# Kernel optimization log

Hardware: AMD Instinct MI355X
Metric: run time of the kernel (lower is better)

## Reference

```python
import jax, jax.numpy as jnp
import numpy as np

HIDDEN = 1024
HEADS = 16
HEAD_DIM = HIDDEN // HEADS
B, L = 2, 2048
EPS = 1e-5


def setup_inputs() -> dict:
    key = jax.random.key(0)
    ks = jax.random.split(key, 16)
    s = 0.02
    inp = {
        "hidden_state": jax.random.normal(ks[0], (B, L, HIDDEN), jnp.float32),
        "uncertainty_embedding": jax.random.normal(ks[1], (B, HIDDEN), jnp.float32),
        "attention_mask": jnp.ones((B, L), jnp.int32),
        # projection weights stored (in, out): y = x @ W + b
        "Wq": jax.random.normal(ks[2], (HIDDEN, HIDDEN), jnp.float32) * s,
        "bq": jnp.zeros((HIDDEN,), jnp.float32),
        "Wk": jax.random.normal(ks[3], (HIDDEN, HIDDEN), jnp.float32) * s,
        "bk": jnp.zeros((HIDDEN,), jnp.float32),
        "Wv": jax.random.normal(ks[4], (HIDDEN, HIDDEN), jnp.float32) * s,
        "bv": jnp.zeros((HIDDEN,), jnp.float32),
        "Wo": jax.random.normal(ks[5], (HIDDEN, HIDDEN), jnp.float32) * s,
        "bo": jnp.zeros((HIDDEN,), jnp.float32),
        # uncertainty_scale MLP: hidden -> hidden//4 -> num_heads
        "Wu1": jax.random.normal(ks[6], (HIDDEN, HIDDEN // 4), jnp.float32) * s,
        "bu1": jnp.zeros((HIDDEN // 4,), jnp.float32),
        "Wu2": jax.random.normal(ks[7], (HIDDEN // 4, HEADS), jnp.float32) * s,
        "bu2": jnp.zeros((HEADS,), jnp.float32),
        # LayerNorm
        "gamma": jnp.ones((HIDDEN,), jnp.float32),
        "beta": jnp.zeros((HIDDEN,), jnp.float32),
    }
    return inp


def _forward(hidden_state, uncertainty_embedding, attention_mask,
             Wq, bq, Wk, bk, Wv, bv, Wo, bo, Wu1, bu1, Wu2, bu2, gamma, beta):
    Bb, Ll, _ = hidden_state.shape
    # projections -> (B, H, L, Dh)
    def split_heads(x):
        return x.reshape(Bb, Ll, HEADS, HEAD_DIM).transpose(0, 2, 1, 3)
    Q = split_heads(hidden_state @ Wq + bq)
    K = split_heads(hidden_state @ Wk + bk)
    V = split_heads(hidden_state @ Wv + bv)

    scores = jnp.einsum('bhqd,bhkd->bhqk', Q, K) / (HEAD_DIM ** 0.5)
    mask = (attention_mask == 0)[:, None, None, :]  # (B,1,1,L) over key dim
    scores = jnp.where(mask, -1e9, scores)

    # per-head uncertainty gate in (0,1)
    u = jax.nn.relu(uncertainty_embedding @ Wu1 + bu1)
    scale = jax.nn.sigmoid(u @ Wu2 + bu2)  # (B, H)
    scores = scores * scale[:, :, None, None]

    attn = jax.nn.softmax(scores, axis=-1)
    out = jnp.einsum('bhqk,bhkd->bhqd', attn, V)
    out = out.transpose(0, 2, 1, 3).reshape(Bb, Ll, HIDDEN)
    out = out @ Wo + bo

    y = hidden_state + out
    mu = jnp.mean(y, axis=-1, keepdims=True)
    var = jnp.var(y, axis=-1, keepdims=True)
    return (y - mu) * jax.lax.rsqrt(var + EPS) * gamma + beta


def reference(hidden_state, uncertainty_embedding, attention_mask,
              Wq, bq, Wk, bk, Wv, bv, Wo, bo, Wu1, bu1, Wu2, bu2, gamma, beta):
    return _forward(hidden_state, uncertainty_embedding, attention_mask,
                    Wq, bq, Wk, bk, Wv, bv, Wo, bo, Wu1, bu1, Wu2, bu2, gamma, beta)
```

## Files before the change

### kernel.cpp

```cpp
#include <hip/hip_runtime.h>
#include <hip/hip_bf16.h>

#define HID 1024
#define NHEADS 16
#define DH 64
#define BB 2
#define LL 2048
#define MM (BB*LL)
#define EPSF 1e-5f

typedef __attribute__((ext_vector_type(8))) short bf16x8;
typedef __attribute__((ext_vector_type(4))) float f32x4;

#define MFMA16(A,Bf,C) __builtin_amdgcn_mfma_f32_16x16x32_bf16(A,Bf,C,0,0,0)
#define GLOAD_LDS16(G, Ld) \
  __builtin_amdgcn_global_load_lds((__attribute__((address_space(1))) const void*)(G), \
                                   (__attribute__((address_space(3))) void*)(Ld), 16, 0, 0)
#define PIN(v) asm("" : "+v"(v))
#define EXP2R(x) ({ float _y; asm("v_exp_f32 %0, %1" : "=v"(_y) : "v"(x)); _y; })
#define WAIT_VM0_BAR() do { \
    asm volatile("s_waitcnt vmcnt(0)" ::: "memory"); \
    __builtin_amdgcn_s_barrier(); \
    __builtin_amdgcn_sched_barrier(0); \
  } while (0)

__device__ __forceinline__ unsigned short f2bf(float f) {
  union { float f; unsigned int u; } x; x.f = f;
  unsigned int r = x.u + 0x7fffu + ((x.u >> 16) & 1u);
  return (unsigned short)(r >> 16);
}

__global__ __launch_bounds__(256) void u1_partial(const float* __restrict__ ue,
                                                  const float* __restrict__ Wu1,
                                                  float* __restrict__ upart) {
  int b = blockIdx.y, kb = blockIdx.x;
  __shared__ float su[128];
  int tid = threadIdx.x;
  if (tid < 128) su[tid] = ue[b*HID + kb*128 + tid];
  __syncthreads();
  float s = 0.f;
  const float* w = Wu1 + (size_t)(kb*128)*256 + tid;
  for (int k = 0; k < 128; ++k) s += su[k] * w[(size_t)k*256];
  upart[(b*8 + kb)*256 + tid] = s;
}

__global__ __launch_bounds__(256) void u2_scale(const float* __restrict__ upart,
                                                const float* __restrict__ bu1,
                                                const float* __restrict__ Wu2,
                                                const float* __restrict__ bu2,
                                                float* __restrict__ scale) {
  int b = blockIdx.x, tid = threadIdx.x;
  __shared__ float su[256];
  float s = 0.f;
  for (int kb = 0; kb < 8; ++kb) s += upart[(b*8 + kb)*256 + tid];
  su[tid] = fmaxf(s + bu1[tid], 0.f);
  __syncthreads();
  if (tid < 16) {
    float a = bu2[tid];
    for (int k = 0; k < 256; ++k) a += su[k] * Wu2[k*16 + tid];
    scale[b*NHEADS + tid] = 1.f / (1.f + __expf(-a));
  }
}

__global__ __launch_bounds__(256) void maskprep_kernel(const int* __restrict__ amask,
                                                       const float* __restrict__ scale,
                                                       float* __restrict__ maskf) {
  int i = blockIdx.x*256 + threadIdx.x;
  int base = i*8;
  int bh = base >> 11;
  int b  = bh >> 4;
  float cm = scale[bh] * 1.44269504f;
  int k = base & (LL-1);
  #pragma unroll
  for (int j = 0; j < 8; ++j)
    maskf[base + j] = (amask[b*LL + k + j] == 0 ? -1e9f : 0.f) * cm - 16.f;
}

__global__ __launch_bounds__(256) void convert_x_kernel(const float* __restrict__ X,
                                                        unsigned short* __restrict__ Xb) {
  int i = blockIdx.x*256 + threadIdx.x;
  float4 v = ((const float4*)X)[i];
  ushort4 o; o.x = f2bf(v.x); o.y = f2bf(v.y); o.z = f2bf(v.z); o.w = f2bf(v.w);
  ((ushort4*)Xb)[i] = o;
}

__global__ void transw_kernel(const float* __restrict__ Wq, const float* __restrict__ Wk,
                              const float* __restrict__ Wv, const float* __restrict__ Wo,
                              unsigned short* __restrict__ Wqkvt, unsigned short* __restrict__ Wot) {
  __shared__ float tile[32][33];
  int z = blockIdx.z;
  const float* W = (z==0) ? Wq : (z==1) ? Wk : (z==2) ? Wv : Wo;
  unsigned short* dst = (z < 3) ? (Wqkvt + (size_t)z*HID*HID) : Wot;
  int n0 = blockIdx.x*32, k0 = blockIdx.y*32;
  int tx = threadIdx.x, ty = threadIdx.y;
  #pragma unroll
  for (int i = 0; i < 4; ++i) tile[ty+8*i][tx] = W[(size_t)(k0+ty+8*i)*HID + n0+tx];
  __syncthreads();
  #pragma unroll
  for (int i = 0; i < 4; ++i) dst[(size_t)(n0+ty+8*i)*HID + k0+tx] = f2bf(tile[tx][ty+8*i]);
}

template<int MODE>
__global__ __launch_bounds__(256) void gemm_kernel(
    const unsigned short* __restrict__ A,
    const unsigned short* __restrict__ Bt,
    const float* __restrict__ bias0, const float* __restrict__ bias1, const float* __restrict__ bias2,
    const float* __restrict__ resid,
    unsigned short* __restrict__ outQKV,
    float* __restrict__ outY) {
  constexpr int BM = (MODE == 0) ? 128 : 64;
  constexpr int MI = BM / 32;
  constexpr int ASZ = BM*64*2;
  constexpr int BSZ = 128*64*2;
  __shared__ alignas(16) unsigned short sA[2*BM*64];
  __shared__ alignas(16) unsigned short sB[2*128*64];
  const int tid = threadIdx.x, lane = tid & 63, wv = tid >> 6;
  const int wr = wv >> 1, wc = wv & 1;
  const int bid = blockIdx.x, xcd = bid & 7, loc = bid >> 3;
  const int nIdx = (MODE == 0) ? (xcd*3 + loc % 3) : xcd;
  const int mIdx = (MODE == 0) ? (loc / 3) : loc;
  const int m0 = mIdx*BM, n0 = nIdx*128;
  const int r = lane & 15, g = lane >> 4;

  const unsigned short* pA[MI];
  const unsigned short* pB[4];
  int ldsA[MI], ldsB[4];
  #pragma unroll
  for (int c = 0; c < MI; ++c) {
    const int base = c*4096 + wv*1024;
    const int po = base + lane*16;
    const int uo = po ^ (((po>>7)&7)<<4);
    const int e  = uo >> 1;
    pA[c] = A + (size_t)(m0 + (e>>6))*HID + (e&63);
    ldsA[c] = base;
  }
  #pragma unroll
  for (int c = 0; c < 4; ++c) {
    const int base = c*4096 + wv*1024;
    const int po = base + lane*16;
    const int uo = po ^ (((po>>7)&7)<<4);
    const int e  = uo >> 1;
    pB[c] = Bt + (size_t)(n0 + (e>>6))*HID + (e&63);
    ldsB[c] = base;
  }
  const int sw = (r & 7) << 4;
  int oALo = (wr*(MI*16) + r)*128 + ((g*16) ^ sw);
  int oAHi = (wr*(MI*16) + r)*128 + ((64 + g*16) ^ sw);
  int oBLo = (wc*64 + r)*128 + ((g*16) ^ sw);
  int oBHi = (wc*64 + r)*128 + ((64 + g*16) ^ sw);
  PIN(oALo); PIN(oAHi); PIN(oBLo); PIN(oBHi);

#define GSTAGE(BUF) do {                                                      \
    _Pragma("unroll")                                                         \
    for (int c = 0; c < MI; ++c) {                                            \
      GLOAD_LDS16(pA[c], (char*)sA + (BUF)*ASZ + ldsA[c]); pA[c] += 64;       \
    }                                                                         \
    _Pragma("unroll")                                                         \
    for (int c = 0; c < 4; ++c) {                                             \
      GLOAD_LDS16(pB[c], (char*)sB + (BUF)*BSZ + ldsB[c]); pB[c] += 64;       \
    }                                                                         \
  } while (0)

#define GCOMPUTE(BUF) do {                                                    \
    _Pragma("unroll")                                                         \
    for (int kk = 0; kk < 2; ++kk) {                                          \
      bf16x8 af[MI], bfv[4];                                                  \
      _Pragma("unroll")                                                       \
      for (int i = 0; i < MI; ++i)                                            \
        af[i]  = *(const bf16x8*)((const char*)sA + (BUF)*ASZ +               \
                                  (kk ? oAHi : oALo) + i*2048);               \
      _Pragma("unroll")                                                       \
      for (int j = 0; j < 4; ++j)                                             \
        bfv[j] = *(const bf16x8*)((const char*)sB + (BUF)*BSZ +               \
                                  (kk ? oBHi : oBLo) + j*2048);               \
      __builtin_amdgcn_s_setprio(1);                                          \
      _Pragma("unroll")                                                       \
      for (int i = 0; i < MI; ++i)                                            \
        _Pragma("unroll")                                                     \
        for (int j = 0; j < 4; ++j)                                           \
          acc[i][j] = MFMA16(af[i], bfv[j], acc[i][j]);                       \
      __builtin_amdgcn_s_setprio(0);                                          \
    }                                                                         \
  } while (0)

  f32x4 acc[MI][4];
  #pragma unroll
  for (int i = 0; i < MI; ++i)
    #pragma unroll
    for (int j = 0; j < 4; ++j) acc[i][j] = (f32x4){0.f,0.f,0.f,0.f};

  GSTAGE(0);
  for (int k0 = 0; k0 < HID; k0 += 128) {
    WAIT_VM0_BAR();
    GSTAGE(1);
    GCOMPUTE(0);
    WAIT_VM0_BAR();
    if (k0 + 128 < HID) GSTAGE(0);
    GCOMPUTE(1);
  }
#undef GSTAGE
#undef GCOMPUTE

  if (MODE == 0) {
    const int which = n0 >> 10;
    const float* bias = (which==0) ? bias0 : (which==1) ? bias1 : bias2;
    if (which < 2) {
      unsigned short* dst = outQKV + (size_t)which * ((size_t)MM*HID);
      #pragma unroll
      for (int i = 0; i < MI; ++i)
        #pragma unroll
        for (int j = 0; j < 4; ++j)
          #pragma unroll
          for (int rr = 0; rr < 4; ++rr) {
            int row = m0 + wr*(MI*16) + i*16 + g*4 + rr;
            int col = n0 + wc*64 + j*16 + r;
            int nn = col & (HID-1);
            int hh = nn >> 6, d = nn & 63;
            int bI = row >> 11, l = row & (LL-1);
            float v = acc[i][j][rr] + bias[nn];
            dst[(((size_t)(bI*NHEADS + hh)*LL + l) << 6) + d] = f2bf(v);
          }
    } else {
      unsigned short* dst = outQKV + 2*((size_t)MM*HID);
      #pragma unroll
      for (int i = 0; i < MI; ++i)
        #pragma unroll
        for (int j = 0; j < 4; ++j) {
          int col = n0 + wc*64 + j*16 + r;
          int nn = col & (HID-1);
          int hh = nn >> 6, d = nn & 63;
          int row0 = m0 + wr*(MI*16) + i*16 + g*4;
          int bI = row0 >> 11, l0 = row0 & (LL-1);
          ushort4 o4;
          o4.x = f2bf(acc[i][j][0] + bias[nn]);
          o4.y = f2bf(acc[i][j][1] + bias[nn]);
          o4.z = f2bf(acc[i][j][2] + bias[nn]);
          o4.w = f2bf(acc[i][j][3] + bias[nn]);
          *(ushort4*)(dst + ((size_t)((bI*NHEADS + hh)*DH + d))*LL + l0) = o4;
        }
    }
  } else {
    #pragma unroll
    for (int i = 0; i < MI; ++i)
      #pragma unroll
      for (int j = 0; j < 4; ++j)
        #pragma unroll
        for (int rr = 0; rr < 4; ++rr) {
          int row = m0 + wr*(MI*16) + i*16 + g*4 + rr;
          int col = n0 + wc*64 + j*16 + r;
          size_t idx = (size_t)row*HID + col;
          outY[idx] = acc[i][j][rr] + bias0[col] + resid[idx];
        }
  }
}

__global__ __launch_bounds__(256, 4) void attn_kernel(
    const unsigned short* __restrict__ Qb,
    const unsigned short* __restrict__ Kb,
    const unsigned short* __restrict__ Vt,
    const float* __restrict__ maskf,
    const float* __restrict__ scale_ws,
    unsigned short* __restrict__ attnout) {
  __shared__ alignas(16) unsigned short sK[2*64*64];
  __shared__ alignas(16) unsigned short sV[2*64*64];
  __shared__ alignas(16) unsigned short sP[4][16*64];
  const int p = blockIdx.x;
  const int bh = (p & 7)*4 + ((p >> 3) >> 5);
  const int q0 = ((p >> 3) & 31) * 64;
  const int b  = bh >> 4;
  const int tid = threadIdx.x, lane = tid & 63, wv = tid >> 6;
  const int r = lane & 15, g = lane >> 4;
  const size_t hoff = (size_t)bh * (LL*DH);
  const float c2 = 0.125f * scale_ws[bh] * 1.44269504f;
  const unsigned short* Kg = Kb + hoff;
  const unsigned short* Vg = Vt + hoff;
  const float* pm = maskf + (size_t)bh*LL + g*4;

  const unsigned short* pKs[2];
  const unsigned short* pVs[2];
  int lbase[2];
  #pragma unroll
  for (int c = 0; c < 2; ++c) {
    const int base_ = c*4096 + wv*1024;
    const int po_ = base_ + lane*16;
    const int uo_ = po_ ^ (((po_>>7)&7)<<4);
    const int e_  = uo_ >> 1;
    pKs[c] = Kg + (size_t)(e_>>6)*DH + (e_&63);
    pVs[c] = Vg + (size_t)(e_>>6)*LL + (e_&63);
    lbase[c] = base_;
  }

  const int sw = (r & 7) << 4;
  int oLo = r*128 + ((g*16) ^ sw);
  int oHi = r*128 + ((64 + g*16) ^ sw);
  PIN(oLo); PIN(oHi);
  int wP[4];
  #pragma unroll
  for (int kt = 0; kt < 4; ++kt) {
    wP[kt] = r*128 + ((kt*32 + g*8) ^ sw);
    PIN(wP[kt]);
  }

  bf16x8 aQ[2];
  {
    const int qrow = q0 + wv*16 + r;
    #pragma unroll
    for (int kc = 0; kc < 2; ++kc)
      aQ[kc] = *(const bf16x8*)(Qb + hoff + (size_t)qrow*DH + kc*32 + g*8);
  }
  const short ONE_BF = (short)0x3F80;
  const bf16x8 vone = {ONE_BF,ONE_BF,ONE_BF,ONE_BF,ONE_BF,ONE_BF,ONE_BF,ONE_BF};

  f32x4 accO[4];
  #pragma unroll
  for (int j = 0; j < 4; ++j) accO[j] = (f32x4){0.f,0.f,0.f,0.f};
  f32x4 lsum = (f32x4){0.f,0.f,0.f,0.f};

  #pragma unroll
  for (int c = 0; c < 2; ++c) {
    GLOAD_LDS16(pKs[c], (char*)sK + lbase[c]);
    GLOAD_LDS16(pVs[c], (char*)sV + lbase[c]);
    pKs[c] += 64*DH;  pVs[c] += 64;
  }
  float4 mreg[4];
  #pragma unroll
  for (int kt = 0; kt < 4; ++kt) mreg[kt] = *(const float4*)(pm + kt*16);
  pm += 64;

#define ATILE(CUROFF, NBOFF, T) do {                                          \
    WAIT_VM0_BAR();                            \
    if ((T) + 1 < LL/64) {                     \
      _Pragma("unroll")                                                       \
      for (int c = 0; c < 2; ++c) {                                           \
        GLOAD_LDS16(pKs[c], (char*)sK + (NBOFF) + lbase[c]);                  \
        GLOAD_LDS16(pVs[c], (char*)sV + (NBOFF) + lbase[c]);                  \
        pKs[c] += 64*DH;  pVs[c] += 64;                                       \
      }                                                                       \
    }                                                                         \
    f32x4 sc[4];                                                              \
    __builtin_amdgcn_s_setprio(1);                                            \
    _Pragma("unroll")                                                         \
    for (int kt = 0; kt < 4; ++kt) {                                          \
      bf16x8 bk0 = *(const bf16x8*)((const char*)sK + (CUROFF) + oLo + kt*2048); \
      bf16x8 bk1 = *(const bf16x8*)((const char*)sK + (CUROFF) + oHi + kt*2048); \
      f32x4 a = (f32x4){0.f,0.f,0.f,0.f};                                     \
      a = MFMA16(bk0, aQ[0], a);                                              \
      a = MFMA16(bk1, aQ[1], a);                                              \
      sc[kt] = a;                                                             \
    }                                                                         \
    __builtin_amdgcn_s_setprio(0);                                            \
    _Pragma("unroll")                                                         \
    for (int kt = 0; kt < 4; ++kt) {                                          \
      sc[kt][0] = EXP2R(sc[kt][0]*c2 + mreg[kt].x);                           \
      sc[kt][1] = EXP2R(sc[kt][1]*c2 + mreg[kt].y);                           \
      sc[kt][2] = EXP2R(sc[kt][2]*c2 + mreg[kt].z);                           \
      sc[kt][3] = EXP2R(sc[kt][3]*c2 + mreg[kt].w);                           \
    }                                                                         \
    if ((T) + 1 < LL/64) {                                                    \
      _Pragma("unroll")                                                       \
      for (int kt = 0; kt < 4; ++kt) mreg[kt] = *(const float4*)(pm + kt*16); \
      pm += 64;                                                               \
    }                                                                         \
    char* sPw = (char*)sP[wv];                                                \
    _Pragma("unroll")                                                         \
    for (int kt = 0; kt < 4; ++kt) {                                          \
      unsigned int lo, hi;                                                    \
      asm("v_cvt_pk_bf16_f32 %0, %1, %2" : "=v"(lo) : "v"(sc[kt][0]), "v"(sc[kt][1])); \
      asm("v_cvt_pk_bf16_f32 %0, %1, %2" : "=v"(hi) : "v"(sc[kt][2]), "v"(sc[kt][3])); \
      uint2 w; w.x = lo; w.y = hi;                                            \
      *(uint2*)(sPw + wP[kt]) = w;                                            \
    }                                                                         \
    bf16x8 aP0 = *(const bf16x8*)(sPw + oLo);                                 \
    bf16x8 aP1 = *(const bf16x8*)(sPw + oHi);                                 \
    lsum = MFMA16(vone, aP0, lsum);                                           \
    lsum = MFMA16(vone, aP1, lsum);                                           \
    __builtin_amdgcn_s_setprio(1);                                            \
    _Pragma("unroll")                                                         \
    for (int j = 0; j < 4; ++j) {                                             \
      bf16x8 v0 = *(const bf16x8*)((const char*)sV + (CUROFF) + oLo + j*2048); \
      bf16x8 v1 = *(const bf16x8*)((const char*)sV + (CUROFF) + oHi + j*2048); \
      accO[j] = MFMA16(v0, aP0, accO[j]);                                     \
      accO[j] = MFMA16(v1, aP1, accO[j]);                                     \
    }                                                                         \
    __builtin_amdgcn_s_setprio(0);                                            \
  } while (0)

  for (int t = 0; t < LL/64; t += 2) {
    ATILE(0,    8192, t);
    ATILE(8192, 0,    t+1);
  }
#undef ATILE

  const float invl = 1.f / lsum[0];
  const int qq = q0 + wv*16 + r;
  #pragma unroll
  for (int j = 0; j < 4; ++j) {
    ushort4 o4;
    o4.x = f2bf(accO[j][0] * invl);
    o4.y = f2bf(accO[j][1] * invl);
    o4.z = f2bf(accO[j][2] * invl);
    o4.w = f2bf(accO[j][3] * invl);
    const int col = (bh & 15)*DH + j*16 + g*4;
    *(ushort4*)(attnout + (size_t)(b*LL + qq)*HID + col) = o4;
  }
}

__global__ __launch_bounds__(256) void ln_kernel(const float* __restrict__ Y,
                                                 const float* __restrict__ gamma,
                                                 const float* __restrict__ beta,
                                                 float* __restrict__ out) {
  int row = blockIdx.x, tid = threadIdx.x;
  const float* y = Y + (size_t)row*HID;
  float v[4]; float s = 0.f, s2 = 0.f;
  #pragma unroll
  for (int i = 0; i < 4; ++i) { v[i] = y[tid + i*256]; s += v[i]; s2 += v[i]*v[i]; }
  #pragma unroll
  for (int o = 1; o < 64; o <<= 1) { s += __shfl_xor(s, o, 64); s2 += __shfl_xor(s2, o, 64); }
  __shared__ float ws1[4], ws2[4];
  if ((tid & 63) == 0) { ws1[tid>>6] = s; ws2[tid>>6] = s2; }
  __syncthreads();
  s  = ws1[0] + ws1[1] + ws1[2] + ws1[3];
  s2 = ws2[0] + ws2[1] + ws2[2] + ws2[3];
  float mu  = s * (1.f/HID);
  float var = s2 * (1.f/HID) - mu*mu;
  float rs  = rsqrtf(var + EPSF);
  #pragma unroll
  for (int i = 0; i < 4; ++i) {
    int c = tid + i*256;
    out[(size_t)row*HID + c] = (v[i] - mu)*rs*gamma[c] + beta[c];
  }
}

extern "C" void kernel_launch(void* const* d_in, const int* in_sizes, int n_in,
                              void* d_out, int out_size, void* d_ws, size_t ws_size,
                              hipStream_t stream) {
  const float* hidden = (const float*)d_in[0];
  const float* ue     = (const float*)d_in[1];
  const int*   amask  = (const int*)d_in[2];
  const float* Wq = (const float*)d_in[3];  const float* bq = (const float*)d_in[4];
  const float* Wk = (const float*)d_in[5];  const float* bk = (const float*)d_in[6];
  const float* Wv = (const float*)d_in[7];  const float* bv = (const float*)d_in[8];
  const float* Wo = (const float*)d_in[9];  const float* bo = (const float*)d_in[10];
  const float* Wu1 = (const float*)d_in[11]; const float* bu1 = (const float*)d_in[12];
  const float* Wu2 = (const float*)d_in[13]; const float* bu2 = (const float*)d_in[14];
  const float* gamma = (const float*)d_in[15]; const float* beta = (const float*)d_in[16];
  float* out = (float*)d_out;

  char* ws = (char*)d_ws;
  if (ws_size < ((56u<<20) + 32768)) return;
  unsigned short* Xbf   = (unsigned short*)(ws + 0);
  float*          Y     = (float*)(ws + 0);
  float*          maskf = (float*)(ws + (8u<<20));
  unsigned short* Wqkvt = (unsigned short*)(ws + (16u<<20));
  unsigned short* Wot   = (unsigned short*)(ws + (22u<<20));
  unsigned short* Qb    = (unsigned short*)(ws + (24u<<20));
  unsigned short* Kb    = Qb + (size_t)MM*HID;
  unsigned short* Vb    = Kb + (size_t)MM*HID;
  unsigned short* AOut  = (unsigned short*)(ws + (48u<<20));
  float* upart = (float*)(ws + (56u<<20));
  float* scale = upart + BB*8*256;

  u1_partial<<<dim3(8, BB), 256, 0, stream>>>(ue, Wu1, upart);
  u2_scale<<<BB, 256, 0, stream>>>(upart, bu1, Wu2, bu2, scale);
  maskprep_kernel<<<(BB*NHEADS*LL/8)/256, 256, 0, stream>>>(amask, scale, maskf);
  convert_x_kernel<<<(MM*HID/4)/256, 256, 0, stream>>>(hidden, Xbf);
  transw_kernel<<<dim3(32, 32, 4), dim3(32, 8), 0, stream>>>(Wq, Wk, Wv, Wo, Wqkvt, Wot);
  gemm_kernel<0><<<768, 256, 0, stream>>>(Xbf, Wqkvt,
                                          bq, bk, bv, nullptr, Qb, nullptr);
  attn_kernel<<<BB*NHEADS*(LL/64), 256, 0, stream>>>(Qb, Kb, Vb, maskf, scale, AOut);
  gemm_kernel<1><<<512, 256, 0, stream>>>(AOut, Wot,
                                          bo, nullptr, nullptr, hidden, nullptr, Y);
  ln_kernel<<<MM, 256, 0, stream>>>(Y, gamma, beta, out);
}
```

Before: 144.8 us.

## Split attention key tile across waves and feed P directly from registers

Each wave now handles 16 keys of the 64-key tile for all 64 queries, instead of all keys for its own 16 queries. Because the score accumulator layout from the QK MFMA matches the B operand of the 16x16x16 MFMA, P is fed to the PV MFMA straight from registers. This removes the shared-memory P round-trip and the ones-vector MFMA used for row sums. In exchange, the row sums and output accumulators need a multi-barrier cross-wave reduction through LDS at the end, and register pressure grows (launch bounds drop from 4 to 3 blocks per SM).

```diff
diff --git a/kernel.cpp b/kernel.cpp
--- a/kernel.cpp
+++ b/kernel.cpp
@@ -10,9 +10,11 @@
 #define EPSF 1e-5f
 
 typedef __attribute__((ext_vector_type(8))) short bf16x8;
+typedef __attribute__((ext_vector_type(4))) short bf16x4;
 typedef __attribute__((ext_vector_type(4))) float f32x4;
 
 #define MFMA16(A,Bf,C) __builtin_amdgcn_mfma_f32_16x16x32_bf16(A,Bf,C,0,0,0)
+#define MFMA16K16(A,Bf,C) __builtin_amdgcn_mfma_f32_16x16x16bf16_1k(A,Bf,C,0,0,0)
 #define GLOAD_LDS16(G, Ld) \
   __builtin_amdgcn_global_load_lds((__attribute__((address_space(1))) const void*)(G), \
                                    (__attribute__((address_space(3))) void*)(Ld), 16, 0, 0)
@@ -254,7 +256,7 @@
   }
 }
 
-__global__ __launch_bounds__(256, 4) void attn_kernel(
+__global__ __launch_bounds__(256, 3) void attn_kernel(
     const unsigned short* __restrict__ Qb,
     const unsigned short* __restrict__ Kb,
     const unsigned short* __restrict__ Vt,
@@ -263,7 +265,6 @@
     unsigned short* __restrict__ attnout) {
   __shared__ alignas(16) unsigned short sK[2*64*64];
   __shared__ alignas(16) unsigned short sV[2*64*64];
-  __shared__ alignas(16) unsigned short sP[4][16*64];
   const int p = blockIdx.x;
   const int bh = (p & 7)*4 + ((p >> 3) >> 5);
   const int q0 = ((p >> 3) & 31) * 64;
@@ -274,7 +275,7 @@
   const float c2 = 0.125f * scale_ws[bh] * 1.44269504f;
   const unsigned short* Kg = Kb + hoff;
   const unsigned short* Vg = Vt + hoff;
-  const float* pm = maskf + (size_t)bh*LL + g*4;
+  const float* pm = maskf + (size_t)bh*LL + wv*16 + g*4;
 
   const unsigned short* pKs[2];
   const unsigned short* pVs[2];
@@ -291,30 +292,28 @@
   }
 
   const int sw = (r & 7) << 4;
-  int oLo = r*128 + ((g*16) ^ sw);
-  int oHi = r*128 + ((64 + g*16) ^ sw);
-  PIN(oLo); PIN(oHi);
-  int wP[4];
-  #pragma unroll
-  for (int kt = 0; kt < 4; ++kt) {
-    wP[kt] = r*128 + ((kt*32 + g*8) ^ sw);
-    PIN(wP[kt]);
-  }
-
-  bf16x8 aQ[2];
-  {
-    const int qrow = q0 + wv*16 + r;
+  int oKlo = (wv*16 + r)*128 + ((g*16) ^ sw);
+  int oKhi = (wv*16 + r)*128 + ((64 + g*16) ^ sw);
+  int oVb  = r*128 + ((wv*32 + g*8) ^ sw);
+  PIN(oKlo); PIN(oKhi); PIN(oVb);
+
+  bf16x8 aQ[4][2];
+  #pragma unroll
+  for (int qg = 0; qg < 4; ++qg) {
+    const int qrow = q0 + qg*16 + r;
     #pragma unroll
     for (int kc = 0; kc < 2; ++kc)
-      aQ[kc] = *(const bf16x8*)(Qb + hoff + (size_t)qrow*DH + kc*32 + g*8);
-  }
-  const short ONE_BF = (short)0x3F80;
-  const bf16x8 vone = {ONE_BF,ONE_BF,ONE_BF,ONE_BF,ONE_BF,ONE_BF,ONE_BF,ONE_BF};
-
-  f32x4 accO[4];
-  #pragma unroll
-  for (int j = 0; j < 4; ++j) accO[j] = (f32x4){0.f,0.f,0.f,0.f};
-  f32x4 lsum = (f32x4){0.f,0.f,0.f,0.f};
+      aQ[qg][kc] = *(const bf16x8*)(Qb + hoff + (size_t)qrow*DH + kc*32 + g*8);
+  }
+
+  f32x4 accO[4][4];
+  float lp[4];
+  #pragma unroll
+  for (int qg = 0; qg < 4; ++qg) {
+    lp[qg] = 0.f;
+    #pragma unroll
+    for (int j = 0; j < 4; ++j) accO[qg][j] = (f32x4){0.f,0.f,0.f,0.f};
+  }
 
   #pragma unroll
   for (int c = 0; c < 2; ++c) {
@@ -322,10 +321,7 @@
     GLOAD_LDS16(pVs[c], (char*)sV + lbase[c]);
     pKs[c] += 64*DH;  pVs[c] += 64;
   }
-  float4 mreg[4];
-  #pragma unroll
-  for (int kt = 0; kt < 4; ++kt) mreg[kt] = *(const float4*)(pm + kt*16);
-  pm += 64;
+  float4 mreg = *(const float4*)pm;  pm += 64;
 
 #define ATILE(CUROFF, NBOFF, T) do {                                          \
     WAIT_VM0_BAR();                            \
@@ -337,51 +333,43 @@
         pKs[c] += 64*DH;  pVs[c] += 64;                                       \
       }                                                                       \
     }                                                                         \
+    bf16x8 kA0 = *(const bf16x8*)((const char*)sK + (CUROFF) + oKlo);         \
+    bf16x8 kA1 = *(const bf16x8*)((const char*)sK + (CUROFF) + oKhi);         \
+    bf16x4 vA[4];                                                             \
+    _Pragma("unroll")                                                         \
+    for (int j = 0; j < 4; ++j)                                               \
+      vA[j] = *(const bf16x4*)((const char*)sV + (CUROFF) + oVb + j*2048);    \
     f32x4 sc[4];                                                              \
     __builtin_amdgcn_s_setprio(1);                                            \
     _Pragma("unroll")                                                         \
-    for (int kt = 0; kt < 4; ++kt) {                                          \
-      bf16x8 bk0 = *(const bf16x8*)((const char*)sK + (CUROFF) + oLo + kt*2048); \
-      bf16x8 bk1 = *(const bf16x8*)((const char*)sK + (CUROFF) + oHi + kt*2048); \
+    for (int qg = 0; qg < 4; ++qg) {                                          \
       f32x4 a = (f32x4){0.f,0.f,0.f,0.f};                                     \
-      a = MFMA16(bk0, aQ[0], a);                                              \
-      a = MFMA16(bk1, aQ[1], a);                                              \
-      sc[kt] = a;                                                             \
+      a = MFMA16(kA0, aQ[qg][0], a);                                          \
+      a = MFMA16(kA1, aQ[qg][1], a);                                          \
+      sc[qg] = a;                                                             \
     }                                                                         \
     __builtin_amdgcn_s_setprio(0);                                            \
-    _Pragma("unroll")                                                         \
-    for (int kt = 0; kt < 4; ++kt) {                                          \
-      sc[kt][0] = EXP2R(sc[kt][0]*c2 + mreg[kt].x);                           \
-      sc[kt][1] = EXP2R(sc[kt][1]*c2 + mreg[kt].y);                           \
-      sc[kt][2] = EXP2R(sc[kt][2]*c2 + mreg[kt].z);                           \
-      sc[kt][3] = EXP2R(sc[kt][3]*c2 + mreg[kt].w);                           \
+    bf16x4 pb[4];                                                             \
+    _Pragma("unroll")                                                         \
+    for (int qg = 0; qg < 4; ++qg) {                                          \
+      float p0 = EXP2R(sc[qg][0]*c2 + mreg.x);                                \
+      float p1 = EXP2R(sc[qg][1]*c2 + mreg.y);                                \
+      float p2 = EXP2R(sc[qg][2]*c2 + mreg.z);                                \
+      float p3 = EXP2R(sc[qg][3]*c2 + mreg.w);                                \
+      lp[qg] += (p0 + p1) + (p2 + p3);                                        \
+      unsigned int lo, hi;                                                    \
+      asm("v_cvt_pk_bf16_f32 %0, %1, %2" : "=v"(lo) : "v"(p0), "v"(p1));      \
+      asm("v_cvt_pk_bf16_f32 %0, %1, %2" : "=v"(hi) : "v"(p2), "v"(p3));      \
+      unsigned int pw[2] = {lo, hi};                                          \
+      pb[qg] = *(bf16x4*)pw;                                                  \
     }                                                                         \
-    if ((T) + 1 < LL/64) {                                                    \
+    if ((T) + 1 < LL/64) { mreg = *(const float4*)pm;  pm += 64; }            \
+    __builtin_amdgcn_s_setprio(1);                                            \
+    _Pragma("unroll")                                                         \
+    for (int qg = 0; qg < 4; ++qg)                                            \
       _Pragma("unroll")                                                       \
-      for (int kt = 0; kt < 4; ++kt) mreg[kt] = *(const float4*)(pm + kt*16); \
-      pm += 64;                                                               \
-    }                                                                         \
-    char* sPw = (char*)sP[wv];                                                \
-    _Pragma("unroll")                                                         \
-    for (int kt = 0; kt < 4; ++kt) {                                          \
-      unsigned int lo, hi;                                                    \
-      asm("v_cvt_pk_bf16_f32 %0, %1, %2" : "=v"(lo) : "v"(sc[kt][0]), "v"(sc[kt][1])); \
-      asm("v_cvt_pk_bf16_f32 %0, %1, %2" : "=v"(hi) : "v"(sc[kt][2]), "v"(sc[kt][3])); \
-      uint2 w; w.x = lo; w.y = hi;                                            \
-      *(uint2*)(sPw + wP[kt]) = w;                                            \
-    }                                                                         \
-    bf16x8 aP0 = *(const bf16x8*)(sPw + oLo);                                 \
-    bf16x8 aP1 = *(const bf16x8*)(sPw + oHi);                                 \
-    lsum = MFMA16(vone, aP0, lsum);                                           \
-    lsum = MFMA16(vone, aP1, lsum);                                           \
-    __builtin_amdgcn_s_setprio(1);                                            \
-    _Pragma("unroll")                                                         \
-    for (int j = 0; j < 4; ++j) {                                             \
-      bf16x8 v0 = *(const bf16x8*)((const char*)sV + (CUROFF) + oLo + j*2048); \
-      bf16x8 v1 = *(const bf16x8*)((const char*)sV + (CUROFF) + oHi + j*2048); \
-      accO[j] = MFMA16(v0, aP0, accO[j]);                                     \
-      accO[j] = MFMA16(v1, aP1, accO[j]);                                     \
-    }                                                                         \
+      for (int j = 0; j < 4; ++j)                                             \
+        accO[qg][j] = MFMA16K16(vA[j], pb[qg], accO[qg][j]);                  \
     __builtin_amdgcn_s_setprio(0);                                            \
   } while (0)
 
@@ -391,17 +379,73 @@
   }
 #undef ATILE
 
-  const float invl = 1.f / lsum[0];
-  const int qq = q0 + wv*16 + r;
-  #pragma unroll
-  for (int j = 0; j < 4; ++j) {
-    ushort4 o4;
-    o4.x = f2bf(accO[j][0] * invl);
-    o4.y = f2bf(accO[j][1] * invl);
-    o4.z = f2bf(accO[j][2] * invl);
-    o4.w = f2bf(accO[j][3] * invl);
-    const int col = (bh & 15)*DH + j*16 + g*4;
-    *(ushort4*)(attnout + (size_t)(b*LL + qq)*HID + col) = o4;
+  #pragma unroll
+  for (int qg = 0; qg < 4; ++qg) {
+    lp[qg] += __shfl_xor(lp[qg], 16, 64);
+    lp[qg] += __shfl_xor(lp[qg], 32, 64);
+  }
+  __syncthreads();
+  float* red1 = (float*)sK;
+  float* red2 = (float*)sV;
+  if (wv > 0 && g == 0) {
+    #pragma unroll
+    for (int qg = 0; qg < 4; ++qg) red1[(wv-1)*64 + qg*16 + r] = lp[qg];
+  }
+  __syncthreads();
+  float invl[4];
+  if (wv == 0) {
+    #pragma unroll
+    for (int qg = 0; qg < 4; ++qg)
+      invl[qg] = 1.f / (lp[qg] + red1[qg*16 + r] + red1[64 + qg*16 + r] + red1[128 + qg*16 + r]);
+  }
+  __syncthreads();
+  if (wv >= 2) {
+    float* dst = (wv == 2) ? red1 : red2;
+    #pragma unroll
+    for (int qg = 0; qg < 4; ++qg)
+      #pragma unroll
+      for (int j = 0; j < 4; ++j)
+        #pragma unroll
+        for (int c = 0; c < 4; ++c)
+          dst[(qg*16 + j*4 + c)*64 + lane] = accO[qg][j][c];
+  }
+  __syncthreads();
+  if (wv < 2) {
+    const float* src = (wv == 0) ? red1 : red2;
+    #pragma unroll
+    for (int qg = 0; qg < 4; ++qg)
+      #pragma unroll
+      for (int j = 0; j < 4; ++j)
+        #pragma unroll
+        for (int c = 0; c < 4; ++c)
+          accO[qg][j][c] += src[(qg*16 + j*4 + c)*64 + lane];
+  }
+  __syncthreads();
+  if (wv == 1) {
+    #pragma unroll
+    for (int qg = 0; qg < 4; ++qg)
+      #pragma unroll
+      for (int j = 0; j < 4; ++j)
+        #pragma unroll
+        for (int c = 0; c < 4; ++c)
+          red1[(qg*16 + j*4 + c)*64 + lane] = accO[qg][j][c];
+  }
+  __syncthreads();
+  if (wv == 0) {
+    #pragma unroll
+    for (int qg = 0; qg < 4; ++qg) {
+      #pragma unroll
+      for (int j = 0; j < 4; ++j) {
+        ushort4 o4;
+        o4.x = f2bf((accO[qg][j][0] + red1[(qg*16 + j*4 + 0)*64 + lane]) * invl[qg]);
+        o4.y = f2bf((accO[qg][j][1] + red1[(qg*16 + j*4 + 1)*64 + lane]) * invl[qg]);
+        o4.z = f2bf((accO[qg][j][2] + red1[(qg*16 + j*4 + 2)*64 + lane]) * invl[qg]);
+        o4.w = f2bf((accO[qg][j][3] + red1[(qg*16 + j*4 + 3)*64 + lane]) * invl[qg]);
+        const int qq = q0 + qg*16 + r;
+        const int col = (bh & 15)*DH + j*16 + g*4;
+        *(ushort4*)(attnout + (size_t)(b*LL + qq)*HID + col) = o4;
+      }
+    }
   }
 }
 
```

New measurement: 166.7 us. 15.1% more time.

## Process two query groups per attention wave to reuse K/V fragments; vectorize LayerNorm

Applied to the files above, without the earlier changes.

The attention kernel moves from 4 waves of 16 query rows each to 2 waves of 32 rows each (128 threads). Each wave reuses the K and V fragments it reads from LDS for two query sub-tiles, which cuts LDS reads per MFMA. The K/V tile loads are spread over four global-to-LDS copies per thread. LayerNorm now uses float4 loads and stores per thread. The trade-off is more registers per wave and fewer waves per block, which may reduce latency hiding.

```diff
diff --git a/kernel.cpp b/kernel.cpp
--- a/kernel.cpp
+++ b/kernel.cpp
@@ -254,7 +254,7 @@
   }
 }
 
-__global__ __launch_bounds__(256, 4) void attn_kernel(
+__global__ __launch_bounds__(128, 2) void attn_kernel(
     const unsigned short* __restrict__ Qb,
     const unsigned short* __restrict__ Kb,
     const unsigned short* __restrict__ Vt,
@@ -263,7 +263,7 @@
     unsigned short* __restrict__ attnout) {
   __shared__ alignas(16) unsigned short sK[2*64*64];
   __shared__ alignas(16) unsigned short sV[2*64*64];
-  __shared__ alignas(16) unsigned short sP[4][16*64];
+  __shared__ alignas(16) unsigned short sP[2][2][16*64];
   const int p = blockIdx.x;
   const int bh = (p & 7)*4 + ((p >> 3) >> 5);
   const int q0 = ((p >> 3) & 31) * 64;
@@ -276,12 +276,12 @@
   const unsigned short* Vg = Vt + hoff;
   const float* pm = maskf + (size_t)bh*LL + g*4;
 
-  const unsigned short* pKs[2];
-  const unsigned short* pVs[2];
-  int lbase[2];
-  #pragma unroll
-  for (int c = 0; c < 2; ++c) {
-    const int base_ = c*4096 + wv*1024;
+  const unsigned short* pKs[4];
+  const unsigned short* pVs[4];
+  int lbase[4];
+  #pragma unroll
+  for (int c = 0; c < 4; ++c) {
+    const int base_ = c*2048 + wv*1024;
     const int po_ = base_ + lane*16;
     const int uo_ = po_ ^ (((po_>>7)&7)<<4);
     const int e_  = uo_ >> 1;
@@ -301,23 +301,28 @@
     PIN(wP[kt]);
   }
 
-  bf16x8 aQ[2];
-  {
-    const int qrow = q0 + wv*16 + r;
+  bf16x8 aQ[2][2];
+  #pragma unroll
+  for (int qg = 0; qg < 2; ++qg) {
+    const int qrow = q0 + wv*32 + qg*16 + r;
     #pragma unroll
     for (int kc = 0; kc < 2; ++kc)
-      aQ[kc] = *(const bf16x8*)(Qb + hoff + (size_t)qrow*DH + kc*32 + g*8);
+      aQ[qg][kc] = *(const bf16x8*)(Qb + hoff + (size_t)qrow*DH + kc*32 + g*8);
   }
   const short ONE_BF = (short)0x3F80;
   const bf16x8 vone = {ONE_BF,ONE_BF,ONE_BF,ONE_BF,ONE_BF,ONE_BF,ONE_BF,ONE_BF};
 
-  f32x4 accO[4];
-  #pragma unroll
-  for (int j = 0; j < 4; ++j) accO[j] = (f32x4){0.f,0.f,0.f,0.f};
-  f32x4 lsum = (f32x4){0.f,0.f,0.f,0.f};
-
-  #pragma unroll
-  for (int c = 0; c < 2; ++c) {
+  f32x4 accO[2][4];
+  f32x4 lsum[2];
+  #pragma unroll
+  for (int qg = 0; qg < 2; ++qg) {
+    lsum[qg] = (f32x4){0.f,0.f,0.f,0.f};
+    #pragma unroll
+    for (int j = 0; j < 4; ++j) accO[qg][j] = (f32x4){0.f,0.f,0.f,0.f};
+  }
+
+  #pragma unroll
+  for (int c = 0; c < 4; ++c) {
     GLOAD_LDS16(pKs[c], (char*)sK + lbase[c]);
     GLOAD_LDS16(pVs[c], (char*)sV + lbase[c]);
     pKs[c] += 64*DH;  pVs[c] += 64;
@@ -331,58 +336,70 @@
     WAIT_VM0_BAR();                            \
     if ((T) + 1 < LL/64) {                     \
       _Pragma("unroll")                                                       \
-      for (int c = 0; c < 2; ++c) {                                           \
+      for (int c = 0; c < 4; ++c) {                                           \
         GLOAD_LDS16(pKs[c], (char*)sK + (NBOFF) + lbase[c]);                  \
         GLOAD_LDS16(pVs[c], (char*)sV + (NBOFF) + lbase[c]);                  \
         pKs[c] += 64*DH;  pVs[c] += 64;                                       \
       }                                                                       \
     }                                                                         \
-    f32x4 sc[4];                                                              \
+    f32x4 sc[2][4];                                                           \
     __builtin_amdgcn_s_setprio(1);                                            \
     _Pragma("unroll")                                                         \
-    for (int kt = 0; kt < 4; ++kt) {                                          \
+    for (int kt = 0; kt < 4; ++kt) {       \
       bf16x8 bk0 = *(const bf16x8*)((const char*)sK + (CUROFF) + oLo + kt*2048); \
       bf16x8 bk1 = *(const bf16x8*)((const char*)sK + (CUROFF) + oHi + kt*2048); \
-      f32x4 a = (f32x4){0.f,0.f,0.f,0.f};                                     \
-      a = MFMA16(bk0, aQ[0], a);                                              \
-      a = MFMA16(bk1, aQ[1], a);                                              \
-      sc[kt] = a;                                                             \
+      _Pragma("unroll")                                                       \
+      for (int qg = 0; qg < 2; ++qg) {                                        \
+        f32x4 a = (f32x4){0.f,0.f,0.f,0.f};                                   \
+        a = MFMA16(bk0, aQ[qg][0], a);                                        \
+        a = MFMA16(bk1, aQ[qg][1], a);                                        \
+        sc[qg][kt] = a;                                                       \
+      }                                                                       \
     }                                                                         \
     __builtin_amdgcn_s_setprio(0);                                            \
     _Pragma("unroll")                                                         \
-    for (int kt = 0; kt < 4; ++kt) {                                          \
-      sc[kt][0] = EXP2R(sc[kt][0]*c2 + mreg[kt].x);                           \
-      sc[kt][1] = EXP2R(sc[kt][1]*c2 + mreg[kt].y);                           \
-      sc[kt][2] = EXP2R(sc[kt][2]*c2 + mreg[kt].z);                           \
-      sc[kt][3] = EXP2R(sc[kt][3]*c2 + mreg[kt].w);                           \
-    }                                                                         \
+    for (int qg = 0; qg < 2; ++qg)                                            \
+      _Pragma("unroll")                                                       \
+      for (int kt = 0; kt < 4; ++kt) {                                        \
+        sc[qg][kt][0] = EXP2R(sc[qg][kt][0]*c2 + mreg[kt].x);                 \
+        sc[qg][kt][1] = EXP2R(sc[qg][kt][1]*c2 + mreg[kt].y);                 \
+        sc[qg][kt][2] = EXP2R(sc[qg][kt][2]*c2 + mreg[kt].z);                 \
+        sc[qg][kt][3] = EXP2R(sc[qg][kt][3]*c2 + mreg[kt].w);                 \
+      }                                                                       \
     if ((T) + 1 < LL/64) {                                                    \
       _Pragma("unroll")                                                       \
       for (int kt = 0; kt < 4; ++kt) mreg[kt] = *(const float4*)(pm + kt*16); \
       pm += 64;                                                               \
     }                                                                         \
-    char* sPw = (char*)sP[wv];                                                \
-    _Pragma("unroll")                                                         \
-    for (int kt = 0; kt < 4; ++kt) {                                          \
-      unsigned int lo, hi;                                                    \
-      asm("v_cvt_pk_bf16_f32 %0, %1, %2" : "=v"(lo) : "v"(sc[kt][0]), "v"(sc[kt][1])); \
-      asm("v_cvt_pk_bf16_f32 %0, %1, %2" : "=v"(hi) : "v"(sc[kt][2]), "v"(sc[kt][3])); \
-      uint2 w; w.x = lo; w.y = hi;                                            \
-      *(uint2*)(sPw + wP[kt]) = w;                                            \
-    }                                                                         \
-    bf16x8 aP0 = *(const bf16x8*)(sPw + oLo);                                 \
-    bf16x8 aP1 = *(const bf16x8*)(sPw + oHi);                                 \
-    lsum = MFMA16(vone, aP0, lsum);                                           \
-    lsum = MFMA16(vone, aP1, lsum);                                           \
-    __builtin_amdgcn_s_setprio(1);                                            \
+    bf16x8 vf0[4], vf1[4];                 \
     _Pragma("unroll")                                                         \
     for (int j = 0; j < 4; ++j) {                                             \
-      bf16x8 v0 = *(const bf16x8*)((const char*)sV + (CUROFF) + oLo + j*2048); \
-      bf16x8 v1 = *(const bf16x8*)((const char*)sV + (CUROFF) + oHi + j*2048); \
-      accO[j] = MFMA16(v0, aP0, accO[j]);                                     \
-      accO[j] = MFMA16(v1, aP1, accO[j]);                                     \
-    }                                                                         \
-    __builtin_amdgcn_s_setprio(0);                                            \
+      vf0[j] = *(const bf16x8*)((const char*)sV + (CUROFF) + oLo + j*2048);   \
+      vf1[j] = *(const bf16x8*)((const char*)sV + (CUROFF) + oHi + j*2048);   \
+    }                                                                         \
+    _Pragma("unroll")                                                         \
+    for (int qg = 0; qg < 2; ++qg) {                                          \
+      char* sPw = (char*)sP[wv][qg];                                          \
+      _Pragma("unroll")                                                       \
+      for (int kt = 0; kt < 4; ++kt) {                                        \
+        unsigned int lo, hi;                                                  \
+        asm("v_cvt_pk_bf16_f32 %0, %1, %2" : "=v"(lo) : "v"(sc[qg][kt][0]), "v"(sc[qg][kt][1])); \
+        asm("v_cvt_pk_bf16_f32 %0, %1, %2" : "=v"(hi) : "v"(sc[qg][kt][2]), "v"(sc[qg][kt][3])); \
+        uint2 w; w.x = lo; w.y = hi;                                          \
+        *(uint2*)(sPw + wP[kt]) = w;                                          \
+      }                                                                       \
+      bf16x8 aP0 = *(const bf16x8*)(sPw + oLo);                               \
+      bf16x8 aP1 = *(const bf16x8*)(sPw + oHi);                               \
+      lsum[qg] = MFMA16(vone, aP0, lsum[qg]);                                 \
+      lsum[qg] = MFMA16(vone, aP1, lsum[qg]);                                 \
+      __builtin_amdgcn_s_setprio(1);                                          \
+      _Pragma("unroll")                                                       \
+      for (int j = 0; j < 4; ++j) {                                           \
+        accO[qg][j] = MFMA16(vf0[j], aP0, accO[qg][j]);                       \
+        accO[qg][j] = MFMA16(vf1[j], aP1, accO[qg][j]);                       \
+      }                                                                       \
+      __builtin_amdgcn_s_setprio(0);                                          \
+    }                                                                         \
   } while (0)
 
   for (int t = 0; t < LL/64; t += 2) {
@@ -391,17 +408,20 @@
   }
 #undef ATILE
 
-  const float invl = 1.f / lsum[0];
-  const int qq = q0 + wv*16 + r;
-  #pragma unroll
-  for (int j = 0; j < 4; ++j) {
-    ushort4 o4;
-    o4.x = f2bf(accO[j][0] * invl);
-    o4.y = f2bf(accO[j][1] * invl);
-    o4.z = f2bf(accO[j][2] * invl);
-    o4.w = f2bf(accO[j][3] * invl);
-    const int col = (bh & 15)*DH + j*16 + g*4;
-    *(ushort4*)(attnout + (size_t)(b*LL + qq)*HID + col) = o4;
+  #pragma unroll
+  for (int qg = 0; qg < 2; ++qg) {
+    const float invl = 1.f / lsum[qg][0];
+    const int qq = q0 + wv*32 + qg*16 + r;
+    #pragma unroll
+    for (int j = 0; j < 4; ++j) {
+      ushort4 o4;
+      o4.x = f2bf(accO[qg][j][0] * invl);
+      o4.y = f2bf(accO[qg][j][1] * invl);
+      o4.z = f2bf(accO[qg][j][2] * invl);
+      o4.w = f2bf(accO[qg][j][3] * invl);
+      const int col = (bh & 15)*DH + j*16 + g*4;
+      *(ushort4*)(attnout + (size_t)(b*LL + qq)*HID + col) = o4;
+    }
   }
 }
 
@@ -410,10 +430,9 @@
                                                  const float* __restrict__ beta,
                                                  float* __restrict__ out) {
   int row = blockIdx.x, tid = threadIdx.x;
-  const float* y = Y + (size_t)row*HID;
-  float v[4]; float s = 0.f, s2 = 0.f;
-  #pragma unroll
-  for (int i = 0; i < 4; ++i) { v[i] = y[tid + i*256]; s += v[i]; s2 += v[i]*v[i]; }
+  const float4 v = ((const float4*)(Y + (size_t)row*HID))[tid];
+  float s  = (v.x + v.y) + (v.z + v.w);
+  float s2 = (v.x*v.x + v.y*v.y) + (v.z*v.z + v.w*v.w);
   #pragma unroll
   for (int o = 1; o < 64; o <<= 1) { s += __shfl_xor(s, o, 64); s2 += __shfl_xor(s2, o, 64); }
   __shared__ float ws1[4], ws2[4];
@@ -424,11 +443,14 @@
   float mu  = s * (1.f/HID);
   float var = s2 * (1.f/HID) - mu*mu;
   float rs  = rsqrtf(var + EPSF);
-  #pragma unroll
-  for (int i = 0; i < 4; ++i) {
-    int c = tid + i*256;
-    out[(size_t)row*HID + c] = (v[i] - mu)*rs*gamma[c] + beta[c];
-  }
+  const float4 gm = ((const float4*)gamma)[tid];
+  const float4 bt = ((const float4*)beta)[tid];
+  float4 o4;
+  o4.x = (v.x - mu)*rs*gm.x + bt.x;
+  o4.y = (v.y - mu)*rs*gm.y + bt.y;
+  o4.z = (v.z - mu)*rs*gm.z + bt.z;
+  o4.w = (v.w - mu)*rs*gm.w + bt.w;
+  ((float4*)(out + (size_t)row*HID))[tid] = o4;
 }
 
 extern "C" void kernel_launch(void* const* d_in, const int* in_sizes, int n_in,
@@ -467,7 +489,7 @@
   transw_kernel<<<dim3(32, 32, 4), dim3(32, 8), 0, stream>>>(Wq, Wk, Wv, Wo, Wqkvt, Wot);
   gemm_kernel<0><<<768, 256, 0, stream>>>(Xbf, Wqkvt,
                                           bq, bk, bv, nullptr, Qb, nullptr);
-  attn_kernel<<<BB*NHEADS*(LL/64), 256, 0, stream>>>(Qb, Kb, Vb, maskf, scale, AOut);
+  attn_kernel<<<BB*NHEADS*(LL/64), 128, 0, stream>>>(Qb, Kb, Vb, maskf, scale, AOut);
   gemm_kernel<1><<<512, 256, 0, stream>>>(AOut, Wot,
                                           bo, nullptr, nullptr, hidden, nullptr, Y);
   ln_kernel<<<MM, 256, 0, stream>>>(Y, gamma, beta, out);
```

Measured after the change: 145.4 us. About the same (+0.5%).
